# Kernel tuning notes

Hardware: AMD Instinct MI355X
Metric: run time of the kernel (lower is better)

The kernel has to match this reference:

```python
import math
import jax, jax.numpy as jnp
import numpy as np

B, DIM, H = 16, 1024, 16
HD = DIM // H                      # 64
P_ORIG = 1024                      # num_patches arg
NP = math.ceil(math.sqrt(P_ORIG)) ** 2 // 2   # 512 attended tokens
ALPHA, BETA, GAMMA = 1.9, 3.8, 15.2           # iRPE euc config, ratio=1.9
NUM_BUCKETS = 2 * int(BETA) + 1               # 7


def _rp_bucket(L):
    """Static euclidean-distance relative-position buckets (iRPE 'euc')."""
    E = int(math.ceil(math.sqrt(L)))
    flat = np.arange(E * E)
    pos = np.stack([flat // E, flat % E], axis=1)[:L].astype(np.float64)  # [L,2]
    diff = pos[:, None, :] - pos[None, :, :]
    dis = np.round(np.sqrt((diff ** 2).sum(-1)))
    far = np.round(ALPHA + np.log(np.maximum(dis, 1e-9) / ALPHA)
                   / math.log(GAMMA / ALPHA) * (BETA - ALPHA))
    idx = np.where(dis <= ALPHA, np.round(dis), np.minimum(far, BETA)).astype(np.int32)
    idx = idx - idx.min()
    return jnp.asarray(idx)  # [L,L] int32 in [0, int(BETA)]

RP_BUCKET = _rp_bucket(NP)


def setup_inputs() -> dict:
    key = jax.random.key(0)
    ks = jax.random.split(key, 7)
    s = 0.02
    return {
        "x": jax.random.normal(ks[0], (B, P_ORIG, DIM), dtype=jnp.float32),
        "wq": jax.random.normal(ks[1], (DIM, DIM), dtype=jnp.float32) * s,
        "wk": jax.random.normal(ks[2], (DIM, DIM), dtype=jnp.float32) * s,
        "wv": jax.random.normal(ks[3], (DIM, DIM), dtype=jnp.float32) * s,
        "rpe_w": jax.random.normal(ks[4], (HD, NUM_BUCKETS), dtype=jnp.float32) * s,
        "proj_w": jax.random.normal(ks[5], (DIM, DIM), dtype=jnp.float32) * s,
        "proj_b": jax.random.normal(ks[6], (DIM,), dtype=jnp.float32) * s,
    }


def reference(x, wq, wk, wv, rpe_w, proj_w, proj_b):
    # F.pad on token axis with pad = NP - N (negative => crop)
    pad = NP - x.shape[1]
    if pad >= 0:
        x = jnp.pad(x, ((0, 0), (0, pad), (0, 0)))
    else:
        x = x[:, :NP, :]
    b = x.shape[0]
    scale = HD ** (-0.5)

    def heads(t):  # [b,NP,DIM] -> [b,H,NP,HD]
        return t.reshape(b, NP, H, HD).transpose(0, 2, 1, 3)

    q = heads(x @ wq.T)
    k = heads(x @ wk.T)
    v = heads(x @ wv.T)

    attn = jnp.einsum('bhid,bhjd->bhij', q, k) * scale
    # contextual RPE on keys (transposed): bias[b,h,i,j] = q[b,h,i,:] . W[:, bucket[i,j]]
    lt = jnp.einsum('bhid,dn->bhin', q, rpe_w)                 # [b,H,NP,NB]
    bias = jnp.take_along_axis(lt, RP_BUCKET[None, None, :, :], axis=3)  # [b,H,NP,NP]
    attn = jax.nn.softmax(attn + bias, axis=-1)

    out = jnp.einsum('bhij,bhjd->bhid', attn, v)
    out = out.transpose(0, 2, 1, 3).reshape(b, NP, DIM)
    out = out @ proj_w.T + proj_b
    return out[:, :P_ORIG, :]
```

## Files before the change

### kernel.cpp

```cpp
#include <hip/hip_runtime.h>

typedef __attribute__((ext_vector_type(8))) __bf16 bf16x8;
typedef __attribute__((ext_vector_type(4))) float f32x4;

#define DEVI static __device__ __forceinline__

DEVI unsigned short f2bf(float f) {
  unsigned int u = __float_as_uint(f);
  u += 0x7fffu + ((u >> 16) & 1u);
  return (unsigned short)(u >> 16);
}
DEVI float bf2f(unsigned short s) {
  return __uint_as_float(((unsigned int)s) << 16);
}

union Frag {
  bf16x8 v;
  __bf16 hf[8];
  unsigned short h[8];
  unsigned int w[4];
};

typedef __attribute__((address_space(1))) const void gv_t;
typedef __attribute__((address_space(3))) void sv_t;
#define GLOAD_LDS16(gp, lp) __builtin_amdgcn_global_load_lds((gv_t*)(gp), (sv_t*)(lp), 16, 0, 0)

#define QSCALE 0.18033688011112042f

__global__ __launch_bounds__(256) void k_prep(
    const float* __restrict__ x, const float* __restrict__ wq,
    const float* __restrict__ wk, const float* __restrict__ wv,
    const float* __restrict__ pw,
    unsigned short* __restrict__ xb, unsigned short* __restrict__ wb,
    unsigned char* __restrict__ bkt)
{
  int t = blockIdx.x * 256 + threadIdx.x;
  if (t >= 1572864) {
    int q = t - 1572864;
    int i = q >> 9, j = q & 511;
    int ir = i / 23, ic = i - ir * 23;
    int jr = j / 23, jc = j - jr * 23;
    int dy = ir - jr, dx = ic - jc;
    double dis = rint(sqrt((double)(dy * dy + dx * dx)));
    int v;
    if (dis <= 1.9) {
      v = (int)rint(dis);
    } else {
      double far = rint(1.9 + log(dis / 1.9) * (1.9 / log(8.0)));
      v = (int)fmin(far, 3.8);
    }
    bkt[q] = (unsigned char)v;
    return;
  }
  const float* src;
  unsigned short* dst;
  if (t < 1048576) {
    long e0 = (long)t << 3;
    int m = (int)(e0 >> 10), cc = (int)(e0 & 1023);
    int b = m >> 9, i = m & 511;
    src = x + (((long)(b << 10) + i) << 10) + cc;
    dst = xb + ((long)m << 10) + cc;
  } else {
    long e0 = (long)(t - 1048576) << 3;
    int mat = (int)(e0 >> 20);
    long off = e0 & 1048575;
    const float* s = (mat == 0) ? wq : (mat == 1) ? wk : (mat == 2) ? wv : pw;
    src = s + off;
    dst = wb + e0;
  }
  float4 a = *(const float4*)src;
  float4 b4 = *(const float4*)(src + 4);
  uint4 o;
  o.x = f2bf(a.x)  | ((unsigned)f2bf(a.y)  << 16);
  o.y = f2bf(a.z)  | ((unsigned)f2bf(a.w)  << 16);
  o.z = f2bf(b4.x) | ((unsigned)f2bf(b4.y) << 16);
  o.w = f2bf(b4.z) | ((unsigned)f2bf(b4.w) << 16);
  *(uint4*)dst = o;
}

__global__ __launch_bounds__(512) void k_gemm8(
    const unsigned short* __restrict__ A,
    const unsigned short* __restrict__ Bw,
    unsigned short* __restrict__ qh, unsigned short* __restrict__ kh,
    unsigned short* __restrict__ vt)
{
  __shared__ unsigned short sL[2 * 28672];

  const int bid = blockIdx.x;
  const int swz = (bid & 7) * 64 + (bid >> 3);
  const int tileN = swz & 15, tileM = swz >> 4;

  const int t = threadIdx.x;
  const int w = t >> 6, lane = t & 63;
  const int g4 = lane >> 4, c = lane & 15;
  const int wm = w >> 2, wn = w & 3;

  const char* lbase = (const char*)sL;
  const int acb = c * 64 + ((g4 * 16) ^ ((c & 8) ? 32 : 0));
  const int aoffbase = wm * 8192 + acb;
  int boff[3][2];
#pragma unroll
  for (int ni = 0; ni < 3; ++ni) {
    int row = wn * 48 + ni * 16 + c;
    int base = 32768 + (row >> 6) * 8192 + (row & 63) * 128;
    int rx = row & 7;
#pragma unroll
    for (int kk = 0; kk < 2; ++kk)
      boff[ni][kk] = base + (((kk * 4 + g4) ^ rx) << 4);
  }

  const int rowa = w * 16 + (lane >> 2);
  const int cola = ((lane & 3) * 8) ^ (((lane >> 2) & 8) ? 16 : 0);
  const unsigned short* sAp = A + (long)(tileM * 256 + rowa) * 1024 + cola;
  char* ldsta = (char*)sL + t * 16;
  const int rowbb = t >> 3;
  const int colbb = ((t & 7) ^ ((t >> 3) & 7)) * 8;
  const unsigned short* sBp = Bw + (long)(tileN * 192 + rowbb) * 1024 + colbb;
  char* ldstb = (char*)sL + 32768 + t * 16;

#define STGA(rh, kh, kn, ob) \
  GLOAD_LDS16(sAp + (long)(kn) * 64 + (rh) * 131072 + (kh) * 32, \
              ldsta + (ob) + (kh) * 16384 + (rh) * 8192)
#define STGB(gg, kn, ob) \
  GLOAD_LDS16(sBp + (long)(kn) * 64 + (gg) * 65536, \
              ldstb + (ob) + (gg) * 8192)

  f32x4 acc[8][3] = {};

  STGA(0, 0, 0, 0); STGA(1, 0, 0, 0);
  STGB(0, 0, 0); STGB(1, 0, 0); STGB(2, 0, 0);
  STGA(0, 1, 0, 0); STGA(1, 1, 0, 0);
  asm volatile("s_waitcnt vmcnt(2)" ::: "memory");
  __builtin_amdgcn_s_barrier();

#define MFMA12(base_, AREG, BREG)                                           \
  do {                                                                      \
    _Pragma("unroll")                                                       \
    for (int mi_ = 0; mi_ < 4; ++mi_)                                       \
      _Pragma("unroll")                                                     \
      for (int ni_ = 0; ni_ < 3; ++ni_)                                     \
        acc[(base_) + mi_][ni_] = __builtin_amdgcn_mfma_f32_16x16x32_bf16(  \
            AREG[mi_], BREG[ni_], acc[(base_) + mi_][ni_], 0, 0, 0);        \
  } while (0)

#pragma unroll 1
  for (int kt = 0; kt < 16; ++kt) {
    const int cb = (kt & 1) ? 57344 : 0;
    const int ob = cb ^ 57344;
    const int kn = (kt < 15) ? kt + 1 : 15;

    bf16x8 aa[4], bbf[3];
#pragma unroll
    for (int q = 0; q < 4; ++q) aa[q] = *(const bf16x8*)(lbase + cb + aoffbase + q * 1024);
#pragma unroll
    for (int ni = 0; ni < 3; ++ni) bbf[ni] = *(const bf16x8*)(lbase + cb + boff[ni][0]);
    STGA(0, 0, kn, ob); STGA(1, 0, kn, ob);
    __builtin_amdgcn_s_barrier();
    asm volatile("s_waitcnt lgkmcnt(0)" ::: "memory");
    __builtin_amdgcn_s_setprio(1);
    MFMA12(0, aa, bbf);
    __builtin_amdgcn_s_setprio(0);
    __builtin_amdgcn_s_barrier();

#pragma unroll
    for (int q = 0; q < 4; ++q) aa[q] = *(const bf16x8*)(lbase + cb + aoffbase + (4 + q) * 1024);
    STGB(0, kn, ob); STGB(1, kn, ob);
    __builtin_amdgcn_s_barrier();
    asm volatile("s_waitcnt lgkmcnt(0)" ::: "memory");
    __builtin_amdgcn_s_setprio(1);
    MFMA12(4, aa, bbf);
    __builtin_amdgcn_s_setprio(0);
    asm volatile("s_waitcnt vmcnt(4)" ::: "memory");
    __builtin_amdgcn_s_barrier();

#pragma unroll
    for (int q = 0; q < 4; ++q) aa[q] = *(const bf16x8*)(lbase + cb + 16384 + aoffbase + q * 1024);
#pragma unroll
    for (int ni = 0; ni < 3; ++ni) bbf[ni] = *(const bf16x8*)(lbase + cb + boff[ni][1]);
    STGB(2, kn, ob); STGA(0, 1, kn, ob);
    __builtin_amdgcn_s_barrier();
    asm volatile("s_waitcnt lgkmcnt(0)" ::: "memory");
    __builtin_amdgcn_s_setprio(1);
    MFMA12(0, aa, bbf);
    __builtin_amdgcn_s_setprio(0);
    __builtin_amdgcn_s_barrier();

#pragma unroll
    for (int q = 0; q < 4; ++q) aa[q] = *(const bf16x8*)(lbase + cb + 16384 + aoffbase + (4 + q) * 1024);
    STGA(1, 1, kn, ob);
    __builtin_amdgcn_s_barrier();
    asm volatile("s_waitcnt lgkmcnt(0)" ::: "memory");
    __builtin_amdgcn_s_setprio(1);
    MFMA12(4, aa, bbf);
    __builtin_amdgcn_s_setprio(0);
    asm volatile("s_waitcnt vmcnt(2)" ::: "memory");
    __builtin_amdgcn_s_barrier();
  }
  asm volatile("s_waitcnt vmcnt(0)" ::: "memory");
#undef MFMA12
#undef STGA
#undef STGB

  const int m0 = tileM * 256 + wm * 128;
  const int n0 = tileN * 192 + wn * 48;
#pragma unroll
  for (int mi = 0; mi < 8; ++mi) {
    int mrow = m0 + mi * 16 + g4 * 4;
    int b = mrow >> 9, i = mrow & 511;
#pragma unroll
    for (int ni = 0; ni < 3; ++ni) {
      int n = n0 + ni * 16 + c;
      int mat = n >> 10;
      int cc = n & 1023;
      int h = cc >> 6, d = cc & 63;
      long bh = (long)(b * 16 + h);
      if (mat == 2) {
        unsigned int w0 = f2bf(acc[mi][ni][0]) | ((unsigned)f2bf(acc[mi][ni][1]) << 16);
        unsigned int w1 = f2bf(acc[mi][ni][2]) | ((unsigned)f2bf(acc[mi][ni][3]) << 16);
        *(uint2*)(vt + (bh * 64 + d) * 512 + i) = make_uint2(w0, w1);
      } else {
        float sc = (mat == 0) ? QSCALE : 1.0f;
        unsigned short* dst = (mat == 0 ? qh : kh) + (bh * 512 + i) * 64 + d;
#pragma unroll
        for (int r = 0; r < 4; ++r)
          dst[(long)r * 64] = f2bf(acc[mi][ni][r] * sc);
      }
    }
  }
}

__global__ __launch_bounds__(512) void k_gemm_proj(
    const unsigned short* __restrict__ A,
    const unsigned short* __restrict__ Bw,
    float* __restrict__ out, const float* __restrict__ bias)
{
  __shared__ unsigned short sL[3 * 12288];

  const int bid = blockIdx.x;
  const int swz = (bid & 7) * 32 + (bid >> 3);
  const int tileN = swz % 8, tileM = swz / 8;

  const int tid = threadIdx.x;
  const int w = tid >> 6, lane = tid & 63;
  const int g = lane >> 4, c = lane & 15;
  const int wm = w >> 1, wn = w & 1;

  const int sk = (g * 8) ^ ((c & 8) ? 16 : 0);
  int offA[4], offB[4];
#pragma unroll
  for (int i = 0; i < 4; ++i) {
    offA[i] = (wm * 4 + i) * 512 + c * 32 + sk;
    offB[i] = 8192 + (wn * 4 + i) * 512 + c * 32 + sk;
  }

  const int colb = ((lane & 3) * 8) ^ ((lane >= 32) ? 16 : 0);
  const unsigned short* gA0 = A  + ((long)(tileM * 256 + w * 32 + (lane >> 2))) * 1024 + colb;
  const unsigned short* gA1 = gA0 + 16 * 1024;
  const unsigned short* gB0 = Bw + ((long)(tileN * 128 + w * 16 + (lane >> 2))) * 1024 + colb;

#define STAGE(ktile, buf) do {                                             \
    const long ko_ = (long)(ktile) * 32;                                   \
    char* base_ = (char*)sL + (buf) * 24576;                               \
    GLOAD_LDS16(gA0 + ko_, base_ + (w * 2) * 1024 + lane * 16);            \
    GLOAD_LDS16(gA1 + ko_, base_ + (w * 2 + 1) * 1024 + lane * 16);        \
    GLOAD_LDS16(gB0 + ko_, base_ + 16384 + w * 1024 + lane * 16);          \
  } while (0)

  f32x4 acc[4][4] = {};

  STAGE(0, 0);
  STAGE(1, 1);

  int rb = 0, wbuf = 2;
  for (int t = 0; t < 32; ++t) {
    asm volatile("s_waitcnt vmcnt(3)" ::: "memory");
    __builtin_amdgcn_s_barrier();
    int kt = t + 2; if (kt > 31) kt = 31;
    STAGE(kt, wbuf);

    const unsigned short* lb = sL + rb * 12288;
    bf16x8 af[4], bf[4];
#pragma unroll
    for (int i = 0; i < 4; ++i) af[i] = *(const bf16x8*)(lb + offA[i]);
#pragma unroll
    for (int i = 0; i < 4; ++i) bf[i] = *(const bf16x8*)(lb + offB[i]);

    __builtin_amdgcn_s_setprio(1);
#pragma unroll
    for (int mi = 0; mi < 4; ++mi)
#pragma unroll
      for (int ni = 0; ni < 4; ++ni)
        acc[mi][ni] = __builtin_amdgcn_mfma_f32_16x16x32_bf16(af[mi], bf[ni], acc[mi][ni], 0, 0, 0);
    __builtin_amdgcn_s_setprio(0);
    asm volatile("s_waitcnt lgkmcnt(0)" ::: "memory");

    rb = (rb == 2) ? 0 : rb + 1;
    wbuf = (wbuf == 2) ? 0 : wbuf + 1;
  }
  asm volatile("s_waitcnt vmcnt(0)" ::: "memory");
#undef STAGE

  const int m0 = tileM * 256 + wm * 64;
  const int n0 = tileN * 128 + wn * 64;
#pragma unroll
  for (int mi = 0; mi < 4; ++mi) {
    int mrow = m0 + mi * 16 + g * 4;
#pragma unroll
    for (int ni = 0; ni < 4; ++ni) {
      int n = n0 + ni * 16 + c;
      float bv = bias[n];
#pragma unroll
      for (int r = 0; r < 4; ++r)
        out[(long)(mrow + r) * 1024 + n] = acc[mi][ni][r] + bv;
    }
  }
}

__global__ __launch_bounds__(512) void k_attn(
    const unsigned short* __restrict__ qh, const unsigned short* __restrict__ kh,
    const unsigned short* __restrict__ vt, const float* __restrict__ rpe,
    const unsigned char* __restrict__ bkt,
    unsigned short* __restrict__ po0, unsigned short* __restrict__ po1,
    float* __restrict__ ls0, float* __restrict__ ls1)
{
  __shared__ char ring[3 * 8192];
  __shared__ float lt_lds[512 * 9];
  const int bid = blockIdx.x;
  const int head = bid >> 1, kvh = bid & 1;
  const int b = head >> 4, h = head & 15;
  const int t = threadIdx.x;
  const int w = t >> 6, lane = t & 63;
  const int g = lane >> 4, c = lane & 15;
  const int qbase = w * 64;
  const int tb0 = kvh * 8;
  const unsigned short* Q = qh + (long)head * 512 * 64;
  const unsigned short* K = kh + (long)head * 512 * 64;
  const unsigned short* V = vt + (long)head * 64 * 512;
  unsigned short* po = kvh ? po1 : po0;
  float* lsp = kvh ? ls1 : ls0;

  const unsigned short* sgp;
  char* sld;
  int sjstep;
  if (t < 256) {
    int row = t >> 3;
    int chunk = (t & 7) ^ (row & 7);
    sgp = K + (long)row * 64 + chunk * 8;
    sld = ring + t * 16;
    sjstep = 64;
  } else {
    int u = t - 256;
    int row = u >> 2;
    int chunk = (u & 3) ^ (row & 3);
    sgp = V + (long)row * 512 + chunk * 8;
    sld = ring + 4096 + u * 16;
    sjstep = 1;
  }

#define STAGE(jt_, slot_) \
  GLOAD_LDS16(sgp + (long)(jt_) * 32 * sjstep, sld + (slot_) * 8192)

  Frag qu[4][2];
#pragma unroll
  for (int it = 0; it < 4; ++it)
#pragma unroll
    for (int kk = 0; kk < 2; ++kk)
      qu[it][kk].v = *(const bf16x8*)(Q + (qbase + it * 16 + c) * 64 + kk * 32 + g * 8);

  STAGE(tb0 + 0, 0);
  STAGE(tb0 + 1, 1);

  float lt[4][7] = {};
#pragma unroll
  for (int kk = 0; kk < 2; ++kk)
#pragma unroll
    for (int tt = 0; tt < 8; ++tt) {
      int d = kk * 32 + g * 8 + tt;
      const float* rr = rpe + d * 7;
      float r0 = rr[0], r1 = rr[1], r2 = rr[2], r3 = rr[3], r4 = rr[4], r5 = rr[5], r6 = rr[6];
#pragma unroll
      for (int it = 0; it < 4; ++it) {
        float qv = bf2f(qu[it][kk].h[tt]);
        lt[it][0] += qv * r0; lt[it][1] += qv * r1; lt[it][2] += qv * r2;
        lt[it][3] += qv * r3; lt[it][4] += qv * r4; lt[it][5] += qv * r5;
        lt[it][6] += qv * r6;
      }
    }
#pragma unroll
  for (int it = 0; it < 4; ++it)
#pragma unroll
    for (int n = 0; n < 7; ++n) {
      float v = lt[it][n];
      v += __shfl_xor(v, 16);
      v += __shfl_xor(v, 32);
      if (g == 0) lt_lds[(qbase + it * 16 + c) * 9 + n] = v * 8.0f;
    }

  int rowb36[4];
  const unsigned char* bktp[4];
#pragma unroll
  for (int it = 0; it < 4; ++it) {
    int row = qbase + it * 16 + c;
    rowb36[it] = row * 36;
    bktp[it] = bkt + (long)row * 512 + g * 8;
  }

  const int jperm = (c >> 2) * 8 + (c & 3);
  int koff[2][2];
#pragma unroll
  for (int jt = 0; jt < 2; ++jt) {
    int jp = jperm + jt * 4;
#pragma unroll
    for (int kk = 0; kk < 2; ++kk)
      koff[jt][kk] = jp * 128 + (((kk * 4 + g) ^ (jp & 7)) << 4);
  }
  int voff[4];
#pragma unroll
  for (int dt = 0; dt < 4; ++dt) {
    int r = dt * 16 + c;
    voff[dt] = 4096 + r * 64 + ((g ^ (r & 3)) << 4);
  }

  f32x4 oacc[4][4] = {};
  float lp[4] = {0.f, 0.f, 0.f, 0.f};

  int rb = 0, wbuf = 2;
#pragma unroll 1
  for (int kt = 0; kt < 8; ++kt) {
    asm volatile("s_waitcnt vmcnt(1)" ::: "memory");
    __builtin_amdgcn_s_barrier();
    int kn = tb0 + ((kt < 6) ? kt + 2 : 7);
    STAGE(kn, wbuf);

    const char* lb = ring + rb * 8192;
    const int jb = (tb0 + kt) * 32;

    Frag kf[2][2];
#pragma unroll
    for (int jt = 0; jt < 2; ++jt)
#pragma unroll
      for (int kk = 0; kk < 2; ++kk)
        kf[jt][kk].v = *(const bf16x8*)(lb + koff[jt][kk]);

    uint2 bb[4];
#pragma unroll
    for (int it = 0; it < 4; ++it)
      bb[it] = *(const uint2*)(bktp[it] + jb);

    f32x4 s[2][4];
#pragma unroll
    for (int jt = 0; jt < 2; ++jt)
#pragma unroll
      for (int it = 0; it < 4; ++it) {
        f32x4 z = {0.f, 0.f, 0.f, 0.f};
        z = __builtin_amdgcn_mfma_f32_16x16x32_bf16(kf[jt][0].v, qu[it][0].v, z, 0, 0, 0);
        s[jt][it] = __builtin_amdgcn_mfma_f32_16x16x32_bf16(kf[jt][1].v, qu[it][1].v, z, 0, 0, 0);
      }

    Frag pfr[4];
#pragma unroll
    for (int it = 0; it < 4; ++it) {
      float ps = 0.f;
#pragma unroll
      for (int jt = 0; jt < 2; ++jt) {
        unsigned int bw = jt ? bb[it].y : bb[it].x;
#pragma unroll
        for (int r = 0; r < 4; ++r) {
          int bno = (bw >> (8 * r)) & 255;
          float bias = *(const float*)((const char*)lt_lds + rowb36[it] + (bno << 2));
          float sv = s[jt][it][r] + bias;
          float p;
          asm("v_exp_f32 %0, %1" : "=v"(p) : "v"(sv));
          ps += p;
          pfr[it].hf[jt * 4 + r] = (__bf16)p;
        }
      }
      lp[it] += ps;
    }

    bf16x8 vf[4];
#pragma unroll
    for (int dt = 0; dt < 4; ++dt)
      vf[dt] = *(const bf16x8*)(lb + voff[dt]);

#pragma unroll
    for (int dt = 0; dt < 4; ++dt)
#pragma unroll
      for (int it = 0; it < 4; ++it)
        oacc[dt][it] = __builtin_amdgcn_mfma_f32_16x16x32_bf16(vf[dt], pfr[it].v, oacc[dt][it], 0, 0, 0);

    asm volatile("s_waitcnt lgkmcnt(0)" ::: "memory");
    rb = (rb == 2) ? 0 : rb + 1;
    wbuf = (wbuf == 2) ? 0 : wbuf + 1;
  }
  asm volatile("s_waitcnt vmcnt(0)" ::: "memory");
#undef STAGE

#pragma unroll
  for (int it = 0; it < 4; ++it) {
    float v = lp[it];
    v += __shfl_xor(v, 16);
    v += __shfl_xor(v, 32);
    if (g == 0) lsp[head * 512 + qbase + it * 16 + c] = v;
  }

#pragma unroll
  for (int dt = 0; dt < 4; ++dt)
#pragma unroll
    for (int it = 0; it < 4; ++it) {
      int irow = qbase + it * 16 + c;
      int d0 = dt * 16 + g * 4;
      unsigned int w0 = f2bf(oacc[dt][it][0]) | ((unsigned)f2bf(oacc[dt][it][1]) << 16);
      unsigned int w1 = f2bf(oacc[dt][it][2]) | ((unsigned)f2bf(oacc[dt][it][3]) << 16);
      *(uint2*)(po + ((long)(b * 512 + irow)) * 1024 + h * 64 + d0) = make_uint2(w0, w1);
    }
}

__global__ __launch_bounds__(256) void k_merge(
    const unsigned short* __restrict__ po1, const float* __restrict__ ls0,
    const float* __restrict__ ls1, unsigned short* __restrict__ ao)
{
  int idx = blockIdx.x * 256 + threadIdx.x;
  int m = idx >> 7;
  int n0 = (idx & 127) << 3;
  int head = (m >> 9) * 16 + (n0 >> 6);
  int i = m & 511;
  float li = 1.0f / (ls0[head * 512 + i] + ls1[head * 512 + i]);
  long off = (long)m * 1024 + n0;
  uint2 a = *(const uint2*)(ao + off);
  uint2 bq = *(const uint2*)(po1 + off);
  unsigned int r[2];
#pragma unroll
  for (int q = 0; q < 2; ++q) {
    unsigned int ua = q ? a.y : a.x, ub = q ? bq.y : bq.x;
    float f0 = (bf2f((unsigned short)(ua & 0xffff)) + bf2f((unsigned short)(ub & 0xffff))) * li;
    float f1 = (bf2f((unsigned short)(ua >> 16)) + bf2f((unsigned short)(ub >> 16))) * li;
    r[q] = f2bf(f0) | ((unsigned)f2bf(f1) << 16);
  }
  uint2 a2 = *(const uint2*)(ao + off + 4);
  uint2 b2 = *(const uint2*)(po1 + off + 4);
  unsigned int r2[2];
#pragma unroll
  for (int q = 0; q < 2; ++q) {
    unsigned int ua = q ? a2.y : a2.x, ub = q ? b2.y : b2.x;
    float f0 = (bf2f((unsigned short)(ua & 0xffff)) + bf2f((unsigned short)(ub & 0xffff))) * li;
    float f1 = (bf2f((unsigned short)(ua >> 16)) + bf2f((unsigned short)(ub >> 16))) * li;
    r2[q] = f2bf(f0) | ((unsigned)f2bf(f1) << 16);
  }
  *(uint4*)(ao + off) = make_uint4(r[0], r[1], r2[0], r2[1]);
}

extern "C" void kernel_launch(void* const* d_in, const int* in_sizes, int n_in,
                              void* d_out, int out_size, void* d_ws, size_t ws_size,
                              hipStream_t stream) {
  const float* x   = (const float*)d_in[0];
  const float* wq  = (const float*)d_in[1];
  const float* wk  = (const float*)d_in[2];
  const float* wv  = (const float*)d_in[3];
  const float* rpe = (const float*)d_in[4];
  const float* pw  = (const float*)d_in[5];
  const float* pb  = (const float*)d_in[6];
  float* out = (float*)d_out;

  char* ws = (char*)d_ws;
  unsigned short* xb  = (unsigned short*)(ws);
  unsigned short* wb  = (unsigned short*)(ws + 16777216);
  unsigned short* qhp = (unsigned short*)(ws + 25165824);
  unsigned short* khp = (unsigned short*)(ws + 41943040);
  unsigned short* vtp = (unsigned short*)(ws + 58720256);
  unsigned char*  bkt = (unsigned char*)(ws + 75497472);
  unsigned short* po0 = xb;
  unsigned short* po1 = (unsigned short*)d_out;
  float* ls0 = (float*)((char*)d_out + 16777216);
  float* ls1 = (float*)((char*)d_out + 17825792);

  k_prep<<<dim3(7168), dim3(256), 0, stream>>>(x, wq, wk, wv, pw, xb, wb, bkt);
  k_gemm8<<<dim3(512), dim3(512), 0, stream>>>(xb, wb, qhp, khp, vtp);
  k_attn<<<dim3(512), dim3(512), 0, stream>>>(qhp, khp, vtp, rpe, bkt, po0, po1, ls0, ls1);
  k_merge<<<dim3(4096), dim3(256), 0, stream>>>(po1, ls0, ls1, po0);
  k_gemm_proj<<<dim3(256), dim3(512), 0, stream>>>(po0, wb + 3 * 1048576, out, pb);
}
```

Measured before the change: 169.1 us.

## Process all keys per block and fuse softmax normalization, dropping merge kernel

Attention blocks now cover the full key range of a head instead of splitting keys across two blocks. Normalization by the row sum happens in the attention epilogue, so the separate merge kernel and the partial outputs and sums written to memory are removed. This halves the attention grid to 256 blocks, reducing parallelism and latency hiding per CU in exchange for less memory traffic and one fewer launch.

Measured after the change: 148.4 us. 1.14x faster.

```diff
diff --git a/kernel.cpp b/kernel.cpp
--- a/kernel.cpp
+++ b/kernel.cpp
@@ -319,25 +319,19 @@
 __global__ __launch_bounds__(512) void k_attn(
     const unsigned short* __restrict__ qh, const unsigned short* __restrict__ kh,
     const unsigned short* __restrict__ vt, const float* __restrict__ rpe,
-    const unsigned char* __restrict__ bkt,
-    unsigned short* __restrict__ po0, unsigned short* __restrict__ po1,
-    float* __restrict__ ls0, float* __restrict__ ls1)
+    const unsigned char* __restrict__ bkt, unsigned short* __restrict__ ao)
 {
   __shared__ char ring[3 * 8192];
   __shared__ float lt_lds[512 * 9];
-  const int bid = blockIdx.x;
-  const int head = bid >> 1, kvh = bid & 1;
+  const int head = blockIdx.x;
   const int b = head >> 4, h = head & 15;
   const int t = threadIdx.x;
   const int w = t >> 6, lane = t & 63;
   const int g = lane >> 4, c = lane & 15;
   const int qbase = w * 64;
-  const int tb0 = kvh * 8;
   const unsigned short* Q = qh + (long)head * 512 * 64;
   const unsigned short* K = kh + (long)head * 512 * 64;
   const unsigned short* V = vt + (long)head * 64 * 512;
-  unsigned short* po = kvh ? po1 : po0;
-  float* lsp = kvh ? ls1 : ls0;
 
   const unsigned short* sgp;
   char* sld;
@@ -367,8 +361,8 @@
     for (int kk = 0; kk < 2; ++kk)
       qu[it][kk].v = *(const bf16x8*)(Q + (qbase + it * 16 + c) * 64 + kk * 32 + g * 8);
 
-  STAGE(tb0 + 0, 0);
-  STAGE(tb0 + 1, 1);
+  STAGE(0, 0);
+  STAGE(1, 1);
 
   float lt[4][7] = {};
 #pragma unroll
@@ -426,14 +420,14 @@
 
   int rb = 0, wbuf = 2;
 #pragma unroll 1
-  for (int kt = 0; kt < 8; ++kt) {
+  for (int kt = 0; kt < 16; ++kt) {
     asm volatile("s_waitcnt vmcnt(1)" ::: "memory");
     __builtin_amdgcn_s_barrier();
-    int kn = tb0 + ((kt < 6) ? kt + 2 : 7);
+    int kn = (kt < 14) ? kt + 2 : 15;
     STAGE(kn, wbuf);
 
     const char* lb = ring + rb * 8192;
-    const int jb = (tb0 + kt) * 32;
+    const int jb = kt * 32;
 
     Frag kf[2][2];
 #pragma unroll
@@ -496,58 +490,24 @@
   asm volatile("s_waitcnt vmcnt(0)" ::: "memory");
 #undef STAGE
 
+  float li[4];
 #pragma unroll
   for (int it = 0; it < 4; ++it) {
     float v = lp[it];
     v += __shfl_xor(v, 16);
     v += __shfl_xor(v, 32);
-    if (g == 0) lsp[head * 512 + qbase + it * 16 + c] = v;
-  }
-
+    li[it] = 1.0f / v;
+  }
 #pragma unroll
   for (int dt = 0; dt < 4; ++dt)
 #pragma unroll
     for (int it = 0; it < 4; ++it) {
       int irow = qbase + it * 16 + c;
       int d0 = dt * 16 + g * 4;
-      unsigned int w0 = f2bf(oacc[dt][it][0]) | ((unsigned)f2bf(oacc[dt][it][1]) << 16);
-      unsigned int w1 = f2bf(oacc[dt][it][2]) | ((unsigned)f2bf(oacc[dt][it][3]) << 16);
-      *(uint2*)(po + ((long)(b * 512 + irow)) * 1024 + h * 64 + d0) = make_uint2(w0, w1);
-    }
-}
-
-__global__ __launch_bounds__(256) void k_merge(
-    const unsigned short* __restrict__ po1, const float* __restrict__ ls0,
-    const float* __restrict__ ls1, unsigned short* __restrict__ ao)
-{
-  int idx = blockIdx.x * 256 + threadIdx.x;
-  int m = idx >> 7;
-  int n0 = (idx & 127) << 3;
-  int head = (m >> 9) * 16 + (n0 >> 6);
-  int i = m & 511;
-  float li = 1.0f / (ls0[head * 512 + i] + ls1[head * 512 + i]);
-  long off = (long)m * 1024 + n0;
-  uint2 a = *(const uint2*)(ao + off);
-  uint2 bq = *(const uint2*)(po1 + off);
-  unsigned int r[2];
-#pragma unroll
-  for (int q = 0; q < 2; ++q) {
-    unsigned int ua = q ? a.y : a.x, ub = q ? bq.y : bq.x;
-    float f0 = (bf2f((unsigned short)(ua & 0xffff)) + bf2f((unsigned short)(ub & 0xffff))) * li;
-    float f1 = (bf2f((unsigned short)(ua >> 16)) + bf2f((unsigned short)(ub >> 16))) * li;
-    r[q] = f2bf(f0) | ((unsigned)f2bf(f1) << 16);
-  }
-  uint2 a2 = *(const uint2*)(ao + off + 4);
-  uint2 b2 = *(const uint2*)(po1 + off + 4);
-  unsigned int r2[2];
-#pragma unroll
-  for (int q = 0; q < 2; ++q) {
-    unsigned int ua = q ? a2.y : a2.x, ub = q ? b2.y : b2.x;
-    float f0 = (bf2f((unsigned short)(ua & 0xffff)) + bf2f((unsigned short)(ub & 0xffff))) * li;
-    float f1 = (bf2f((unsigned short)(ua >> 16)) + bf2f((unsigned short)(ub >> 16))) * li;
-    r2[q] = f2bf(f0) | ((unsigned)f2bf(f1) << 16);
-  }
-  *(uint4*)(ao + off) = make_uint4(r[0], r[1], r2[0], r2[1]);
+      unsigned int w0 = f2bf(oacc[dt][it][0] * li[it]) | ((unsigned)f2bf(oacc[dt][it][1] * li[it]) << 16);
+      unsigned int w1 = f2bf(oacc[dt][it][2] * li[it]) | ((unsigned)f2bf(oacc[dt][it][3] * li[it]) << 16);
+      *(uint2*)(ao + ((long)(b * 512 + irow)) * 1024 + h * 64 + d0) = make_uint2(w0, w1);
+    }
 }
 
 extern "C" void kernel_launch(void* const* d_in, const int* in_sizes, int n_in,
@@ -569,14 +529,10 @@
   unsigned short* khp = (unsigned short*)(ws + 41943040);
   unsigned short* vtp = (unsigned short*)(ws + 58720256);
   unsigned char*  bkt = (unsigned char*)(ws + 75497472);
-  unsigned short* po0 = xb;
-  unsigned short* po1 = (unsigned short*)d_out;
-  float* ls0 = (float*)((char*)d_out + 16777216);
-  float* ls1 = (float*)((char*)d_out + 17825792);
+  unsigned short* aop = xb;
 
   k_prep<<<dim3(7168), dim3(256), 0, stream>>>(x, wq, wk, wv, pw, xb, wb, bkt);
   k_gemm8<<<dim3(512), dim3(512), 0, stream>>>(xb, wb, qhp, khp, vtp);
-  k_attn<<<dim3(512), dim3(512), 0, stream>>>(qhp, khp, vtp, rpe, bkt, po0, po1, ls0, ls1);
-  k_merge<<<dim3(4096), dim3(256), 0, stream>>>(po1, ls0, ls1, po0);
-  k_gemm_proj<<<dim3(256), dim3(512), 0, stream>>>(po0, wb + 3 * 1048576, out, pb);
-}
+  k_attn<<<dim3(256), dim3(512), 0, stream>>>(qhp, khp, vtp, rpe, bkt, aop);
+  k_gemm_proj<<<dim3(256), dim3(512), 0, stream>>>(aop, wb + 3 * 1048576, out, pb);
+}
```
